# Kernel tuning notes

Hardware: AMD Instinct MI355X
Metric: run time of the kernel (lower is better)

Reference implementation:

```python
import jax, jax.numpy as jnp
import numpy as np

ALPHA = 0.2  # LeakyReLU negative slope
NEG_INF = -9e15


def setup_inputs() -> dict:
    key = jax.random.key(0)
    k1, k2, k3, k4 = jax.random.split(key, 4)
    M, N, Fin, Fout = 32, 1024, 128, 128
    h = jax.random.normal(k1, (M, N, Fin), dtype=jnp.float32)
    adj = jax.random.randint(k2, (M, N, N), 0, 2, dtype=jnp.int32)
    W = jax.random.normal(k3, (Fin, Fout), dtype=jnp.float32) * (1.414 * (6.0 / (Fin + Fout)) ** 0.5)
    a = jax.random.normal(k4, (2 * Fout, 1), dtype=jnp.float32) * (1.414 * (6.0 / (2 * Fout + 1)) ** 0.5)
    return {"h": h, "adj": adj, "W": W, "a": a}


def reference(h, adj, W, a):
    # Wh: [M, N, Fout]
    Wh = jnp.einsum('mnf,fo->mno', h, W)
    Fout = W.shape[1]
    # Algebraic decomposition of concat([Wh_i, Wh_j]) @ a:
    # a_input[m,i,j] @ a == Wh[m,i]@a[:Fout] + Wh[m,j]@a[Fout:]
    e_src = Wh @ a[:Fout, 0]   # [M, N]
    e_dst = Wh @ a[Fout:, 0]   # [M, N]
    e = e_src[:, :, None] + e_dst[:, None, :]      # [M, N, N]
    e = jnp.where(e > 0, e, ALPHA * e)             # LeakyReLU
    masked = jnp.where(adj > 0, e, NEG_INF)
    # NOTE: original softmaxes over dim=1 (faithful reproduction)
    attention = jax.nn.softmax(masked, axis=1)
    # dropout is a no-op in eval mode
    h_prime = jnp.einsum('mij,mjo->mio', attention, Wh)
    return jax.nn.elu(h_prime)  # concat=True branch
```

## Files before the change

### kernel.cpp

```cpp
#include <hip/hip_runtime.h>
#include <hip/hip_bf16.h>

typedef __attribute__((ext_vector_type(4))) float f32x4;
typedef __attribute__((ext_vector_type(8))) short short8;

#define ALPHA 0.2f
#define NEG_BIG -9e15f

static __device__ __forceinline__ short f2bf(float f) {
    __hip_bfloat16 b = __float2bfloat16(f);
    return __builtin_bit_cast(short, b);
}

#define MFMA16(A, B, C) __builtin_amdgcn_mfma_f32_16x16x32_bf16((A), (B), (C), 0, 0, 0)

__global__ __launch_bounds__(128) void k00_wsd(const float* __restrict__ W,
                                               const float* __restrict__ a,
                                               float* __restrict__ wsv,
                                               float* __restrict__ wdv) {
    int k = blockIdx.x, t = threadIdx.x;
    float v = W[k * 128 + t];
    float ps = v * a[t];
    float pd = v * a[128 + t];
    #pragma unroll
    for (int d = 1; d < 64; d <<= 1) {
        ps += __shfl_xor(ps, d);
        pd += __shfl_xor(pd, d);
    }
    __shared__ float tmp[4];
    if ((t & 63) == 0) { tmp[(t >> 6) * 2] = ps; tmp[(t >> 6) * 2 + 1] = pd; }
    __syncthreads();
    if (t == 0) { wsv[k] = tmp[0] + tmp[2]; wdv[k] = tmp[1] + tmp[3]; }
}

__global__ __launch_bounds__(256) void k0_wh(const float* __restrict__ h,
                                             const float* __restrict__ W,
                                             const float* __restrict__ wsv,
                                             const float* __restrict__ wdv,
                                             short* __restrict__ whbt,
                                             float* __restrict__ es,
                                             float* __restrict__ ed) {
    __shared__ __align__(16) short Wt[128 * 136];
    __shared__ __align__(16) float lws[128], lwd[128];
    const int tid = threadIdx.x;
    const int m = blockIdx.x >> 3, rt = blockIdx.x & 7;
    const int R0 = rt * 128;
    #pragma unroll 4
    for (int i = 0; i < 64; ++i) {
        int idx = i * 256 + tid;
        int k = idx >> 7, o = idx & 127;
        Wt[o * 136 + k] = f2bf(W[idx]);
    }
    if (tid < 128) { lws[tid] = wsv[tid]; lwd[tid] = wdv[tid]; }
    __syncthreads();
    const int w = tid >> 6, l = tid & 63;
    const int q = l >> 4, c = l & 15;
    const int row0 = R0 + w * 32 + c;
    f32x4 acc[2][8];
    const f32x4 vzero = {0.f, 0.f, 0.f, 0.f};
    #pragma unroll
    for (int i = 0; i < 2; ++i)
        #pragma unroll
        for (int j = 0; j < 8; ++j) acc[i][j] = vzero;
    float esp0 = 0.f, edp0 = 0.f, esp1 = 0.f, edp1 = 0.f;
    const float* hrow0 = h + ((size_t)m * 1024 + row0) * 128;
    const float* hrow1 = hrow0 + 16 * 128;
    #pragma unroll
    for (int kk = 0; kk < 128; kk += 32) {
        const int kb = kk + q * 8;
        f32x4 wsA = *(const f32x4*)&lws[kb], wsB = *(const f32x4*)&lws[kb + 4];
        f32x4 wdA = *(const f32x4*)&lwd[kb], wdB = *(const f32x4*)&lwd[kb + 4];
        f32x4 h0a = *(const f32x4*)(hrow0 + kb), h0b = *(const f32x4*)(hrow0 + kb + 4);
        f32x4 h1a = *(const f32x4*)(hrow1 + kb), h1b = *(const f32x4*)(hrow1 + kb + 4);
        short8 af0, af1;
        #pragma unroll
        for (int e = 0; e < 4; ++e) {
            esp0 += h0a[e] * wsA[e] + h0b[e] * wsB[e];
            edp0 += h0a[e] * wdA[e] + h0b[e] * wdB[e];
            esp1 += h1a[e] * wsA[e] + h1b[e] * wsB[e];
            edp1 += h1a[e] * wdA[e] + h1b[e] * wdB[e];
            af0[e] = f2bf(h0a[e]); af0[e + 4] = f2bf(h0b[e]);
            af1[e] = f2bf(h1a[e]); af1[e + 4] = f2bf(h1b[e]);
        }
        #pragma unroll
        for (int nf = 0; nf < 8; ++nf) {
            short8 bf = *(const short8*)&Wt[(nf * 16 + c) * 136 + kb];
            acc[0][nf] = MFMA16(af0, bf, acc[0][nf]);
            acc[1][nf] = MFMA16(af1, bf, acc[1][nf]);
        }
    }
    {
        float v0 = esp0; v0 += __shfl_xor(v0, 16); v0 += __shfl_xor(v0, 32);
        float u0 = edp0; u0 += __shfl_xor(u0, 16); u0 += __shfl_xor(u0, 32);
        float v1 = esp1; v1 += __shfl_xor(v1, 16); v1 += __shfl_xor(v1, 32);
        float u1 = edp1; u1 += __shfl_xor(u1, 16); u1 += __shfl_xor(u1, 32);
        if (q == 0) {
            es[m * 1024 + row0] = v0;       ed[m * 1024 + row0] = u0;
            es[m * 1024 + row0 + 16] = v1;  ed[m * 1024 + row0 + 16] = u1;
        }
    }
    #pragma unroll
    for (int mf = 0; mf < 2; ++mf) {
        const int rowb = R0 + w * 32 + mf * 16 + q * 4;
        #pragma unroll
        for (int nf = 0; nf < 8; ++nf) {
            const int o = nf * 16 + c;
            size_t base = ((size_t)m * 128 + o) * 1024 + rowb;
            #pragma unroll
            for (int r = 0; r < 4; r += 2) {
                unsigned lo = (unsigned short)f2bf(acc[mf][nf][r]);
                unsigned hi = (unsigned short)f2bf(acc[mf][nf][r + 1]);
                *(unsigned*)(whbt + base + r) = lo | (hi << 16);
            }
        }
    }
}

__global__ __launch_bounds__(256) void k0m_max(const float* __restrict__ es,
                                               float* __restrict__ mall) {
    const int m = blockIdx.x, tid = threadIdx.x;
    float4 v = *(const float4*)&es[m * 1024 + tid * 4];
    float mx = fmaxf(fmaxf(v.x, v.y), fmaxf(v.z, v.w));
    #pragma unroll
    for (int d = 1; d < 64; d <<= 1) mx = fmaxf(mx, __shfl_xor(mx, d));
    __shared__ float t[4];
    if ((tid & 63) == 0) t[tid >> 6] = mx;
    __syncthreads();
    if (tid == 0) mall[m] = fmaxf(fmaxf(t[0], t[1]), fmaxf(t[2], t[3]));
}

__global__ __launch_bounds__(256) void k1_stats(const int* __restrict__ adj,
                                                const float* __restrict__ es,
                                                const float* __restrict__ ed,
                                                const float* __restrict__ mall,
                                                unsigned long long* __restrict__ bits,
                                                float* __restrict__ spart) {
    const int b = blockIdx.x;
    const int m = b >> 6, it = b & 63;
    const int tid = threadIdx.x;
    const int w = tid >> 6, l = tid & 63;
    const int j0 = tid * 4;
    const float Ma = mall[m];
    const float4 edv = *(const float4*)&ed[m * 1024 + j0];
    float ub[4];
    #pragma unroll
    for (int e = 0; e < 4; ++e) {
        float x = Ma + ((const float*)&edv)[e];
        ub[e] = fmaxf(x, ALPHA * x);
    }
    const int4* ap = (const int4*)(adj + ((size_t)m * 1024 + it * 16) * 1024) + tid;
    int4 av[16];
    #pragma unroll
    for (int r = 0; r < 16; ++r) av[r] = ap[(size_t)r * 256];
    unsigned long long* bp = bits + ((size_t)m * 1024 + it * 16) * 16 + w * 4;
    #pragma unroll
    for (int r = 0; r < 16; ++r) {
        unsigned long long b0 = __ballot(av[r].x != 0);
        unsigned long long b1 = __ballot(av[r].y != 0);
        unsigned long long b2 = __ballot(av[r].z != 0);
        unsigned long long b3 = __ballot(av[r].w != 0);
        if (l == 0) {
            ulonglong2 p0, p1;
            p0.x = b0; p0.y = b1; p1.x = b2; p1.y = b3;
            *(ulonglong2*)(bp + (size_t)r * 16) = p0;
            *(ulonglong2*)(bp + (size_t)r * 16 + 2) = p1;
        }
    }
    float sr[4] = {0.f, 0.f, 0.f, 0.f};
    const float* ep = es + m * 1024 + it * 16;
    #pragma unroll
    for (int r = 0; r < 16; ++r) {
        const float esb = ep[r];
        #pragma unroll
        for (int e = 0; e < 4; ++e) {
            float x = esb + ((const float*)&edv)[e];
            float lk = fmaxf(x, ALPHA * x);
            float t = __expf(lk - ub[e]);
            sr[e] += ((&av[r].x)[e] != 0) ? t : 0.f;
        }
    }
    float4 s4; s4.x = sr[0]; s4.y = sr[1]; s4.z = sr[2]; s4.w = sr[3];
    *(float4*)&spart[((size_t)(m * 64 + it)) * 1024 + j0] = s4;
}

__global__ __launch_bounds__(256) void k1b_combine(const float* __restrict__ spart,
                                                   const float* __restrict__ ed,
                                                   const float* __restrict__ mall,
                                                   float* __restrict__ cc,
                                                   float* __restrict__ dinv) {
    const int g = blockIdx.x * 256 + threadIdx.x;
    const int m = g >> 10, j = g & 1023;
    const float* sp = spart + (size_t)m * 64 * 1024 + j;
    float S = 0.f;
    #pragma unroll
    for (int it = 0; it < 64; ++it) S += sp[it * 1024];
    float x = mall[m] + ed[g];
    float ub = fmaxf(x, ALPHA * x);
    bool dead = !(S > 0.f);
    cc[g] = dead ? NEG_BIG : ub;
    dinv[g] = dead ? (1.0f / 1024.0f) : 1.0f / S;
}

__global__ __launch_bounds__(256) void k2_pv(const unsigned long long* __restrict__ bits,
                                             const short* __restrict__ whbt,
                                             const float* __restrict__ es,
                                             const float* __restrict__ ed,
                                             const float* __restrict__ cc,
                                             const float* __restrict__ dinv,
                                             float* __restrict__ out) {
    __shared__ __align__(16) short Bt[2][128 * 40];
    __shared__ __align__(16) float led[1024], lc[1024], ld[1024];
    const int tid = threadIdx.x;
    const int m = blockIdx.x >> 3, rt = blockIdx.x & 7;
    const int R0 = rt * 128;
    for (int i = tid; i < 1024; i += 256) {
        led[i] = ed[m * 1024 + i];
        lc[i] = cc[m * 1024 + i];
        ld[i] = dinv[m * 1024 + i];
    }
    const int w = tid >> 6, l = tid & 63, q = l >> 4, cl = l & 15;
    const int row0 = R0 + w * 32 + cl;
    const float es0 = es[m * 1024 + row0];
    const float es1 = es[m * 1024 + row0 + 16];
    const unsigned long long* bp0 = bits + ((size_t)m * 1024 + row0) * 16;
    const unsigned long long* bp1 = bp0 + 16 * 16;
    f32x4 acc[2][8];
    const f32x4 vzero = {0.f, 0.f, 0.f, 0.f};
    #pragma unroll
    for (int i = 0; i < 2; ++i)
        #pragma unroll
        for (int jx = 0; jx < 8; ++jx) acc[i][jx] = vzero;
    const int so = tid >> 1, sh = tid & 1;
    const short* gsrc = whbt + ((size_t)m * 128 + so) * 1024 + sh * 16;
    short* dst0 = &Bt[0][so * 40 + sh * 16];
    {
        uint4 r0 = *(const uint4*)gsrc;
        uint4 r1 = *(const uint4*)(gsrc + 8);
        *(uint4*)dst0 = r0;
        *(uint4*)(dst0 + 8) = r1;
    }
    __syncthreads();
    int cur = 0;
    ulonglong2 wa0, wb0, wa1, wb1;
    wa0.x = wa0.y = wb0.x = wb0.y = 0ull;
    wa1.x = wa1.y = wb1.x = wb1.y = 0ull;
    #pragma unroll 2
    for (int kt = 0; kt < 32; ++kt) {
        const int jb = kt * 32 + q * 8;
        if ((kt & 7) == 0) {
            const ulonglong2* q0 = (const ulonglong2*)(bp0 + (kt >> 3) * 4);
            wa0 = q0[0]; wb0 = q0[1];
            const ulonglong2* q1 = (const ulonglong2*)(bp1 + (kt >> 3) * 4);
            wa1 = q1[0]; wb1 = q1[1];
        }
        uint4 n0, n1;
        if (kt < 31) {
            const short* g2 = gsrc + (kt + 1) * 32;
            n0 = *(const uint4*)g2;
            n1 = *(const uint4*)(g2 + 8);
        }
        const f32x4 edA = *(const f32x4*)&led[jb], edB = *(const f32x4*)&led[jb + 4];
        const f32x4 cA = *(const f32x4*)&lc[jb],   cB = *(const f32x4*)&lc[jb + 4];
        const f32x4 dA = *(const f32x4*)&ld[jb],   dB = *(const f32x4*)&ld[jb + 4];
        const int bbase = ((kt & 7) << 3) + (q << 1);
        short8 af0, af1;
        #pragma unroll
        for (int e = 0; e < 8; ++e) {
            const float edv = (e < 4) ? edA[e] : edB[e - 4];
            const float cv = (e < 4) ? cA[e] : cB[e - 4];
            const float dv = (e < 4) ? dA[e] : dB[e - 4];
            const float x0 = es0 + edv, x1 = es1 + edv;
            const float l0 = fmaxf(x0, ALPHA * x0), l1 = fmaxf(x1, ALPHA * x1);
            const int bi = bbase + (e >> 2);
            const unsigned long long q0w = (e & 3) == 0 ? wa0.x : (e & 3) == 1 ? wa0.y
                                         : (e & 3) == 2 ? wb0.x : wb0.y;
            const unsigned long long q1w = (e & 3) == 0 ? wa1.x : (e & 3) == 1 ? wa1.y
                                         : (e & 3) == 2 ? wb1.x : wb1.y;
            const float m0 = ((q0w >> bi) & 1ull) ? l0 : NEG_BIG;
            const float m1 = ((q1w >> bi) & 1ull) ? l1 : NEG_BIG;
            af0[e] = f2bf(__expf(m0 - cv) * dv);
            af1[e] = f2bf(__expf(m1 - cv) * dv);
        }
        const short* bb = &Bt[cur][0];
        #pragma unroll
        for (int nf = 0; nf < 8; ++nf) {
            short8 bf = *(const short8*)&bb[(nf * 16 + cl) * 40 + q * 8];
            acc[0][nf] = MFMA16(af0, bf, acc[0][nf]);
            acc[1][nf] = MFMA16(af1, bf, acc[1][nf]);
        }
        if (kt < 31) {
            short* d2 = &Bt[cur ^ 1][so * 40 + sh * 16];
            *(uint4*)d2 = n0;
            *(uint4*)(d2 + 8) = n1;
            cur ^= 1;
        }
        __syncthreads();
    }
    #pragma unroll
    for (int mf = 0; mf < 2; ++mf) {
        const int rowb = R0 + w * 32 + mf * 16 + q * 4;
        #pragma unroll
        for (int nf = 0; nf < 8; ++nf) {
            const int o = nf * 16 + cl;
            #pragma unroll
            for (int r = 0; r < 4; ++r) {
                const float v = acc[mf][nf][r];
                const float evv = v > 0.f ? v : (__expf(v) - 1.0f);
                out[((size_t)m * 1024 + rowb + r) * 128 + o] = evv;
            }
        }
    }
}

extern "C" void kernel_launch(void* const* d_in, const int* in_sizes, int n_in,
                              void* d_out, int out_size, void* d_ws, size_t ws_size,
                              hipStream_t stream) {
    const float* h = (const float*)d_in[0];
    const int* adj = (const int*)d_in[1];
    const float* W = (const float*)d_in[2];
    const float* a = (const float*)d_in[3];
    float* out = (float*)d_out;

    char* p = (char*)d_ws;
    auto alloc = [&](size_t bytes) -> char* {
        char* r = p;
        p += (bytes + 255) & ~(size_t)255;
        return r;
    };
    short* whbt = (short*)alloc((size_t)32 * 128 * 1024 * 2);
    float* es = (float*)alloc((size_t)32 * 1024 * 4);
    float* ed = (float*)alloc((size_t)32 * 1024 * 4);
    float* wsv = (float*)alloc(128 * 4);
    float* wdv = (float*)alloc(128 * 4);
    float* mall = (float*)alloc(32 * 4);
    unsigned long long* bits = (unsigned long long*)alloc((size_t)32 * 1024 * 16 * 8);
    float* spart = (float*)alloc((size_t)32 * 64 * 1024 * 4);
    float* cc = (float*)alloc((size_t)32 * 1024 * 4);
    float* dinv = (float*)alloc((size_t)32 * 1024 * 4);

    k00_wsd<<<128, 128, 0, stream>>>(W, a, wsv, wdv);
    k0_wh<<<256, 256, 0, stream>>>(h, W, wsv, wdv, whbt, es, ed);
    k0m_max<<<32, 256, 0, stream>>>(es, mall);
    k1_stats<<<2048, 256, 0, stream>>>(adj, es, ed, mall, bits, spart);
    k1b_combine<<<128, 256, 0, stream>>>(spart, ed, mall, cc, dinv);
    k2_pv<<<256, 256, 0, stream>>>(bits, whbt, es, ed, cc, dinv, out);
}
```

Before: 89.21 us.

## Split adjacency bit-packing from softmax column-sum computation into separate kernels

The fused stats kernel is split in two. A pure streaming kernel packs the int32 adjacency into bitmasks, 32 rows per block, with loads batched ahead of the ballots. A second kernel recomputes the column exp-sums from the packed bits, 64 rows per block, with es staged in shared memory. Partial sums shrink from 64 to 16 per column, so the combine step does less work. The cost is an extra launch and a re-read of the bitmask (small) in exchange for decoupling the bandwidth-bound pack from the exp-heavy sum.

New measurement: 99.86 us. +11.9%, slower.

```diff
diff --git a/kernel.cpp b/kernel.cpp
--- a/kernel.cpp
+++ b/kernel.cpp
@@ -129,58 +129,73 @@
     if (tid == 0) mall[m] = fmaxf(fmaxf(t[0], t[1]), fmaxf(t[2], t[3]));
 }
 
-__global__ __launch_bounds__(256) void k1_stats(const int* __restrict__ adj,
+__global__ __launch_bounds__(256) void k1a_pack(const int* __restrict__ adj,
+                                                unsigned long long* __restrict__ bits) {
+    const int b = blockIdx.x;
+    const int m = b >> 5, it = b & 31;
+    const int tid = threadIdx.x, w = tid >> 6, l = tid & 63;
+    const int4* ap = (const int4*)(adj + ((size_t)m * 1024 + it * 32) * 1024) + tid;
+    unsigned long long* bp = bits + ((size_t)m * 1024 + it * 32) * 16 + w * 4;
+    #pragma unroll
+    for (int rb = 0; rb < 32; rb += 16) {
+        int4 av[16];
+        #pragma unroll
+        for (int r = 0; r < 16; ++r) av[r] = ap[(size_t)(rb + r) * 256];
+        __builtin_amdgcn_sched_barrier(0);
+        #pragma unroll
+        for (int r = 0; r < 16; ++r) {
+            unsigned long long b0 = __ballot(av[r].x != 0);
+            unsigned long long b1 = __ballot(av[r].y != 0);
+            unsigned long long b2 = __ballot(av[r].z != 0);
+            unsigned long long b3 = __ballot(av[r].w != 0);
+            if (l == 0) {
+                ulonglong2 p0; p0.x = b0; p0.y = b1;
+                ulonglong2 p1; p1.x = b2; p1.y = b3;
+                *(ulonglong2*)(bp + (size_t)(rb + r) * 16) = p0;
+                *(ulonglong2*)(bp + (size_t)(rb + r) * 16 + 2) = p1;
+            }
+        }
+    }
+}
+
+__global__ __launch_bounds__(256) void k1c_sums(const unsigned long long* __restrict__ bits,
                                                 const float* __restrict__ es,
                                                 const float* __restrict__ ed,
                                                 const float* __restrict__ mall,
-                                                unsigned long long* __restrict__ bits,
                                                 float* __restrict__ spart) {
     const int b = blockIdx.x;
-    const int m = b >> 6, it = b & 63;
-    const int tid = threadIdx.x;
-    const int w = tid >> 6, l = tid & 63;
+    const int m = b >> 4, it = b & 15;
+    const int tid = threadIdx.x, w = tid >> 6, l = tid & 63;
     const int j0 = tid * 4;
+    __shared__ float les[64];
+    if (tid < 64) les[tid] = es[m * 1024 + it * 64 + tid];
     const float Ma = mall[m];
     const float4 edv = *(const float4*)&ed[m * 1024 + j0];
-    float ub[4];
+    float ub[4], sr[4] = {0.f, 0.f, 0.f, 0.f};
     #pragma unroll
     for (int e = 0; e < 4; ++e) {
         float x = Ma + ((const float*)&edv)[e];
         ub[e] = fmaxf(x, ALPHA * x);
     }
-    const int4* ap = (const int4*)(adj + ((size_t)m * 1024 + it * 16) * 1024) + tid;
-    int4 av[16];
-    #pragma unroll
-    for (int r = 0; r < 16; ++r) av[r] = ap[(size_t)r * 256];
-    unsigned long long* bp = bits + ((size_t)m * 1024 + it * 16) * 16 + w * 4;
-    #pragma unroll
-    for (int r = 0; r < 16; ++r) {
-        unsigned long long b0 = __ballot(av[r].x != 0);
-        unsigned long long b1 = __ballot(av[r].y != 0);
-        unsigned long long b2 = __ballot(av[r].z != 0);
-        unsigned long long b3 = __ballot(av[r].w != 0);
-        if (l == 0) {
-            ulonglong2 p0, p1;
-            p0.x = b0; p0.y = b1; p1.x = b2; p1.y = b3;
-            *(ulonglong2*)(bp + (size_t)r * 16) = p0;
-            *(ulonglong2*)(bp + (size_t)r * 16 + 2) = p1;
-        }
-    }
-    float sr[4] = {0.f, 0.f, 0.f, 0.f};
-    const float* ep = es + m * 1024 + it * 16;
-    #pragma unroll
-    for (int r = 0; r < 16; ++r) {
-        const float esb = ep[r];
+    const ulonglong2* bp = (const ulonglong2*)(bits + ((size_t)m * 1024 + it * 64) * 16 + w * 4);
+    __syncthreads();
+    #pragma unroll 4
+    for (int i = 0; i < 64; ++i) {
+        ulonglong2 q0 = bp[i * 8];
+        ulonglong2 q1 = bp[i * 8 + 1];
+        const float esb = les[i];
         #pragma unroll
         for (int e = 0; e < 4; ++e) {
+            const unsigned long long wv = (e == 0) ? q0.x : (e == 1) ? q0.y
+                                        : (e == 2) ? q1.x : q1.y;
             float x = esb + ((const float*)&edv)[e];
             float lk = fmaxf(x, ALPHA * x);
             float t = __expf(lk - ub[e]);
-            sr[e] += ((&av[r].x)[e] != 0) ? t : 0.f;
+            sr[e] += ((wv >> l) & 1ull) ? t : 0.f;
         }
     }
     float4 s4; s4.x = sr[0]; s4.y = sr[1]; s4.z = sr[2]; s4.w = sr[3];
-    *(float4*)&spart[((size_t)(m * 64 + it)) * 1024 + j0] = s4;
+    *(float4*)&spart[((size_t)(m * 16 + it)) * 1024 + j0] = s4;
 }
 
 __global__ __launch_bounds__(256) void k1b_combine(const float* __restrict__ spart,
@@ -190,10 +205,10 @@
                                                    float* __restrict__ dinv) {
     const int g = blockIdx.x * 256 + threadIdx.x;
     const int m = g >> 10, j = g & 1023;
-    const float* sp = spart + (size_t)m * 64 * 1024 + j;
+    const float* sp = spart + (size_t)m * 16 * 1024 + j;
     float S = 0.f;
     #pragma unroll
-    for (int it = 0; it < 64; ++it) S += sp[it * 1024];
+    for (int it = 0; it < 16; ++it) S += sp[it * 1024];
     float x = mall[m] + ed[g];
     float ub = fmaxf(x, ALPHA * x);
     bool dead = !(S > 0.f);
@@ -334,14 +349,15 @@
     float* wdv = (float*)alloc(128 * 4);
     float* mall = (float*)alloc(32 * 4);
     unsigned long long* bits = (unsigned long long*)alloc((size_t)32 * 1024 * 16 * 8);
-    float* spart = (float*)alloc((size_t)32 * 64 * 1024 * 4);
+    float* spart = (float*)alloc((size_t)32 * 16 * 1024 * 4);
     float* cc = (float*)alloc((size_t)32 * 1024 * 4);
     float* dinv = (float*)alloc((size_t)32 * 1024 * 4);
 
     k00_wsd<<<128, 128, 0, stream>>>(W, a, wsv, wdv);
     k0_wh<<<256, 256, 0, stream>>>(h, W, wsv, wdv, whbt, es, ed);
     k0m_max<<<32, 256, 0, stream>>>(es, mall);
-    k1_stats<<<2048, 256, 0, stream>>>(adj, es, ed, mall, bits, spart);
+    k1a_pack<<<1024, 256, 0, stream>>>(adj, bits);
+    k1c_sums<<<512, 256, 0, stream>>>(bits, es, ed, mall, spart);
     k1b_combine<<<128, 256, 0, stream>>>(spart, ed, mall, cc, dinv);
     k2_pv<<<256, 256, 0, stream>>>(bits, whbt, es, ed, cc, dinv, out);
 }
```

## Fuse six GAT kernels into one cooperative persistent kernel with grid syncs

Applied to the files above, without the earlier changes.

Replaces the six-kernel chain with a single cooperative kernel of 256 blocks that runs the Wh projection, the adjacency bitmask/column-sum stats and the attention-times-Wh MFMA phase, separated by grid.sync. Each block recomputes W·a, the column max and the combine step locally instead of running separate small kernels. The adj stream now goes through double-buffered global_load_lds. The aim is to remove launch gaps and the small serial kernels. The cost is that the heavy adj-scan phase runs on only 256 blocks instead of 2048, which may cut bandwidth utilisation.

Result: no change. 88.87 us (-0.4%).

```diff
diff --git a/kernel.cpp b/kernel.cpp
--- a/kernel.cpp
+++ b/kernel.cpp
@@ -1,8 +1,12 @@
 #include <hip/hip_runtime.h>
 #include <hip/hip_bf16.h>
+#include <hip/hip_cooperative_groups.h>
+
+namespace cg = cooperative_groups;
 
 typedef __attribute__((ext_vector_type(4))) float f32x4;
 typedef __attribute__((ext_vector_type(8))) short short8;
+typedef __attribute__((ext_vector_type(4))) int i32x4;
 
 #define ALPHA 0.2f
 #define NEG_BIG -9e15f
@@ -13,6 +17,310 @@
 }
 
 #define MFMA16(A, B, C) __builtin_amdgcn_mfma_f32_16x16x32_bf16((A), (B), (C), 0, 0, 0)
+
+struct SA { short Wt[128 * 136]; float la[256]; float lws[128]; float lwd[128]; };
+struct SB { int buf[2][4096]; float les[128]; float red[8]; };
+struct SC { short Bt[2][128 * 40]; float led[1024]; float lc[1024]; float ld[1024]; float red[8]; };
+
+__global__ __launch_bounds__(256) void gat_mega(
+        const float* __restrict__ h, const int* __restrict__ adj,
+        const float* __restrict__ W, const float* __restrict__ a,
+        short* __restrict__ whbt, float* __restrict__ es, float* __restrict__ ed,
+        unsigned long long* __restrict__ bits, float* __restrict__ spart,
+        float* __restrict__ out) {
+    __shared__ __align__(16) char smem[36864];
+    cg::grid_group grid = cg::this_grid();
+    const int b = blockIdx.x;
+    const int tid = threadIdx.x;
+    const int w = tid >> 6, l = tid & 63;
+    const int q = l >> 4, cl = l & 15;
+    const int m = b >> 3, sub = b & 7;
+    const int T0 = sub * 128;
+
+    {
+        SA* S = (SA*)smem;
+        S->la[tid] = a[tid];
+        __syncthreads();
+        {
+            const int k = tid >> 1, hh = tid & 1;
+            const float* wr = W + k * 128 + hh * 64;
+            float ps = 0.f, pd = 0.f;
+            #pragma unroll
+            for (int f = 0; f < 64; f += 4) {
+                f32x4 wv = *(const f32x4*)(wr + f);
+                #pragma unroll
+                for (int e = 0; e < 4; ++e) {
+                    ps += wv[e] * S->la[hh * 64 + f + e];
+                    pd += wv[e] * S->la[128 + hh * 64 + f + e];
+                }
+            }
+            ps += __shfl_xor(ps, 1);
+            pd += __shfl_xor(pd, 1);
+            if (hh == 0) { S->lws[k] = ps; S->lwd[k] = pd; }
+        }
+        #pragma unroll 4
+        for (int i = 0; i < 64; ++i) {
+            int idx = i * 256 + tid;
+            int kk = idx >> 7, o = idx & 127;
+            S->Wt[o * 136 + kk] = f2bf(W[idx]);
+        }
+        __syncthreads();
+        const int row0 = T0 + w * 32 + cl;
+        f32x4 acc[2][8];
+        const f32x4 vz = {0.f, 0.f, 0.f, 0.f};
+        #pragma unroll
+        for (int i = 0; i < 2; ++i)
+            #pragma unroll
+            for (int j = 0; j < 8; ++j) acc[i][j] = vz;
+        float esp0 = 0.f, edp0 = 0.f, esp1 = 0.f, edp1 = 0.f;
+        const float* hrow0 = h + ((size_t)m * 1024 + row0) * 128;
+        const float* hrow1 = hrow0 + 16 * 128;
+        #pragma unroll
+        for (int kk = 0; kk < 128; kk += 32) {
+            const int kb = kk + q * 8;
+            f32x4 wsA = *(const f32x4*)&S->lws[kb], wsB = *(const f32x4*)&S->lws[kb + 4];
+            f32x4 wdA = *(const f32x4*)&S->lwd[kb], wdB = *(const f32x4*)&S->lwd[kb + 4];
+            f32x4 h0a = *(const f32x4*)(hrow0 + kb), h0b = *(const f32x4*)(hrow0 + kb + 4);
+            f32x4 h1a = *(const f32x4*)(hrow1 + kb), h1b = *(const f32x4*)(hrow1 + kb + 4);
+            short8 af0, af1;
+            #pragma unroll
+            for (int e = 0; e < 4; ++e) {
+                esp0 += h0a[e] * wsA[e] + h0b[e] * wsB[e];
+                edp0 += h0a[e] * wdA[e] + h0b[e] * wdB[e];
+                esp1 += h1a[e] * wsA[e] + h1b[e] * wsB[e];
+                edp1 += h1a[e] * wdA[e] + h1b[e] * wdB[e];
+                af0[e] = f2bf(h0a[e]); af0[e + 4] = f2bf(h0b[e]);
+                af1[e] = f2bf(h1a[e]); af1[e + 4] = f2bf(h1b[e]);
+            }
+            #pragma unroll
+            for (int nf = 0; nf < 8; ++nf) {
+                short8 bf = *(const short8*)&S->Wt[(nf * 16 + cl) * 136 + kb];
+                acc[0][nf] = MFMA16(af0, bf, acc[0][nf]);
+                acc[1][nf] = MFMA16(af1, bf, acc[1][nf]);
+            }
+        }
+        {
+            float v0 = esp0; v0 += __shfl_xor(v0, 16); v0 += __shfl_xor(v0, 32);
+            float u0 = edp0; u0 += __shfl_xor(u0, 16); u0 += __shfl_xor(u0, 32);
+            float v1 = esp1; v1 += __shfl_xor(v1, 16); v1 += __shfl_xor(v1, 32);
+            float u1 = edp1; u1 += __shfl_xor(u1, 16); u1 += __shfl_xor(u1, 32);
+            if (q == 0) {
+                es[m * 1024 + row0] = v0;       ed[m * 1024 + row0] = u0;
+                es[m * 1024 + row0 + 16] = v1;  ed[m * 1024 + row0 + 16] = u1;
+            }
+        }
+        #pragma unroll
+        for (int mf = 0; mf < 2; ++mf) {
+            const int rowb = T0 + w * 32 + mf * 16 + q * 4;
+            #pragma unroll
+            for (int nf = 0; nf < 8; ++nf) {
+                const int o = nf * 16 + cl;
+                size_t base = ((size_t)m * 128 + o) * 1024 + rowb;
+                #pragma unroll
+                for (int r = 0; r < 4; r += 2) {
+                    unsigned lo = (unsigned short)f2bf(acc[mf][nf][r]);
+                    unsigned hi = (unsigned short)f2bf(acc[mf][nf][r + 1]);
+                    *(unsigned*)(whbt + base + r) = lo | (hi << 16);
+                }
+            }
+        }
+    }
+    __threadfence();
+    grid.sync();
+
+    {
+        SB* S = (SB*)smem;
+        {
+            f32x4 ev = *(const f32x4*)&es[m * 1024 + tid * 4];
+            float mx = fmaxf(fmaxf(ev[0], ev[1]), fmaxf(ev[2], ev[3]));
+            #pragma unroll
+            for (int d = 1; d < 64; d <<= 1) mx = fmaxf(mx, __shfl_xor(mx, d));
+            if (l == 0) S->red[w] = mx;
+        }
+        const size_t gr2 = (size_t)m * 1024 + T0;
+        if (tid < 128) S->les[tid] = es[gr2 + tid];
+        __syncthreads();
+        const float Ma = fmaxf(fmaxf(S->red[0], S->red[1]), fmaxf(S->red[2], S->red[3]));
+        const int j0 = tid * 4;
+        const f32x4 edv = *(const f32x4*)&ed[m * 1024 + j0];
+        float ub[4], sr[4] = {0.f, 0.f, 0.f, 0.f};
+        #pragma unroll
+        for (int e = 0; e < 4; ++e) {
+            float x = Ma + edv[e];
+            ub[e] = fmaxf(x, ALPHA * x);
+        }
+        auto issue = [&](int s) {
+            const int row = s * 4 + w;
+            const int* gp = adj + (gr2 + row) * 1024 + l * 4;
+            int* dst = &S->buf[s & 1][w * 1024];
+            #pragma unroll
+            for (int k = 0; k < 4; ++k)
+                __builtin_amdgcn_global_load_lds(
+                    (const __attribute__((address_space(1))) void*)(gp + k * 256),
+                    (__attribute__((address_space(3))) void*)(dst + k * 256), 16, 0, 0);
+        };
+        issue(0);
+        #pragma unroll 1
+        for (int s = 0; s < 32; ++s) {
+            if (s < 31) {
+                issue(s + 1);
+                asm volatile("s_waitcnt vmcnt(16)" ::: "memory");
+            } else {
+                asm volatile("s_waitcnt vmcnt(0)" ::: "memory");
+            }
+            __builtin_amdgcn_s_barrier();
+            const int* bufc = S->buf[s & 1];
+            unsigned long long* bprow = bits + (gr2 + (size_t)s * 4) * 16 + w * 4;
+            #pragma unroll
+            for (int r = 0; r < 4; ++r) {
+                const i32x4 av = *(const i32x4*)&bufc[r * 1024 + j0];
+                unsigned long long b0 = __ballot(av[0] != 0);
+                unsigned long long b1 = __ballot(av[1] != 0);
+                unsigned long long b2 = __ballot(av[2] != 0);
+                unsigned long long b3 = __ballot(av[3] != 0);
+                if (l == 0) {
+                    ulonglong2 p0; p0.x = b0; p0.y = b1;
+                    ulonglong2 p1; p1.x = b2; p1.y = b3;
+                    *(ulonglong2*)(bprow + (size_t)r * 16) = p0;
+                    *(ulonglong2*)(bprow + (size_t)r * 16 + 2) = p1;
+                }
+                const float esb = S->les[s * 4 + r];
+                #pragma unroll
+                for (int e = 0; e < 4; ++e) {
+                    float x = esb + edv[e];
+                    float lk = fmaxf(x, ALPHA * x);
+                    float t = __expf(lk - ub[e]);
+                    sr[e] += (av[e] != 0) ? t : 0.f;
+                }
+            }
+            __builtin_amdgcn_s_barrier();
+        }
+        f32x4 s4; s4[0] = sr[0]; s4[1] = sr[1]; s4[2] = sr[2]; s4[3] = sr[3];
+        *(f32x4*)&spart[((size_t)(m * 8 + sub)) * 1024 + j0] = s4;
+    }
+    __threadfence();
+    grid.sync();
+
+    {
+        SC* S = (SC*)smem;
+        {
+            f32x4 ev = *(const f32x4*)&es[m * 1024 + tid * 4];
+            float mx = fmaxf(fmaxf(ev[0], ev[1]), fmaxf(ev[2], ev[3]));
+            #pragma unroll
+            for (int d = 1; d < 64; d <<= 1) mx = fmaxf(mx, __shfl_xor(mx, d));
+            if (l == 0) S->red[w] = mx;
+        }
+        __syncthreads();
+        const float Ma = fmaxf(fmaxf(S->red[0], S->red[1]), fmaxf(S->red[2], S->red[3]));
+        const int j0 = tid * 4;
+        {
+            f32x4 Sv = {0.f, 0.f, 0.f, 0.f};
+            const float* sp = spart + (size_t)m * 8 * 1024 + j0;
+            #pragma unroll
+            for (int it = 0; it < 8; ++it) Sv += *(const f32x4*)(sp + it * 1024);
+            f32x4 edv4 = *(const f32x4*)&ed[m * 1024 + j0];
+            #pragma unroll
+            for (int e = 0; e < 4; ++e) {
+                float x = Ma + edv4[e];
+                float ubv = fmaxf(x, ALPHA * x);
+                bool dead = !(Sv[e] > 0.f);
+                S->led[j0 + e] = edv4[e];
+                S->lc[j0 + e] = dead ? NEG_BIG : ubv;
+                S->ld[j0 + e] = dead ? (1.0f / 1024.0f) : 1.0f / Sv[e];
+            }
+        }
+        const int row0 = T0 + w * 32 + cl;
+        const float es0 = es[m * 1024 + row0];
+        const float es1 = es[m * 1024 + row0 + 16];
+        const unsigned long long* bp0 = bits + ((size_t)m * 1024 + row0) * 16;
+        const unsigned long long* bp1 = bp0 + 16 * 16;
+        f32x4 acc[2][8];
+        const f32x4 vz = {0.f, 0.f, 0.f, 0.f};
+        #pragma unroll
+        for (int i = 0; i < 2; ++i)
+            #pragma unroll
+            for (int jx = 0; jx < 8; ++jx) acc[i][jx] = vz;
+        const int so = tid >> 1, sh = tid & 1;
+        const short* gsrc = whbt + ((size_t)m * 128 + so) * 1024 + sh * 16;
+        short* dst0 = &S->Bt[0][so * 40 + sh * 16];
+        {
+            uint4 r0 = *(const uint4*)gsrc;
+            uint4 r1 = *(const uint4*)(gsrc + 8);
+            *(uint4*)dst0 = r0;
+            *(uint4*)(dst0 + 8) = r1;
+        }
+        __syncthreads();
+        int cur = 0;
+        ulonglong2 wa0, wb0, wa1, wb1;
+        wa0.x = wa0.y = wb0.x = wb0.y = 0ull;
+        wa1.x = wa1.y = wb1.x = wb1.y = 0ull;
+        #pragma unroll 2
+        for (int kt = 0; kt < 32; ++kt) {
+            const int jb = kt * 32 + q * 8;
+            if ((kt & 7) == 0) {
+                const ulonglong2* q0p = (const ulonglong2*)(bp0 + (kt >> 3) * 4);
+                wa0 = q0p[0]; wb0 = q0p[1];
+                const ulonglong2* q1p = (const ulonglong2*)(bp1 + (kt >> 3) * 4);
+                wa1 = q1p[0]; wb1 = q1p[1];
+            }
+            uint4 n0, n1;
+            if (kt < 31) {
+                const short* g2 = gsrc + (kt + 1) * 32;
+                n0 = *(const uint4*)g2;
+                n1 = *(const uint4*)(g2 + 8);
+            }
+            const f32x4 edA = *(const f32x4*)&S->led[jb], edB = *(const f32x4*)&S->led[jb + 4];
+            const f32x4 cA = *(const f32x4*)&S->lc[jb],   cB = *(const f32x4*)&S->lc[jb + 4];
+            const f32x4 dA = *(const f32x4*)&S->ld[jb],   dB = *(const f32x4*)&S->ld[jb + 4];
+            const int bbase = ((kt & 7) << 3) + (q << 1);
+            short8 af0, af1;
+            #pragma unroll
+            for (int e = 0; e < 8; ++e) {
+                const float edvv = (e < 4) ? edA[e] : edB[e - 4];
+                const float cv = (e < 4) ? cA[e] : cB[e - 4];
+                const float dv = (e < 4) ? dA[e] : dB[e - 4];
+                const float x0 = es0 + edvv, x1 = es1 + edvv;
+                const float l0 = fmaxf(x0, ALPHA * x0), l1 = fmaxf(x1, ALPHA * x1);
+                const int bi = bbase + (e >> 2);
+                const unsigned long long q0w = (e & 3) == 0 ? wa0.x : (e & 3) == 1 ? wa0.y
+                                             : (e & 3) == 2 ? wb0.x : wb0.y;
+                const unsigned long long q1w = (e & 3) == 0 ? wa1.x : (e & 3) == 1 ? wa1.y
+                                             : (e & 3) == 2 ? wb1.x : wb1.y;
+                const float m0 = ((q0w >> bi) & 1ull) ? l0 : NEG_BIG;
+                const float m1 = ((q1w >> bi) & 1ull) ? l1 : NEG_BIG;
+                af0[e] = f2bf(__expf(m0 - cv) * dv);
+                af1[e] = f2bf(__expf(m1 - cv) * dv);
+            }
+            #pragma unroll
+            for (int nf = 0; nf < 8; ++nf) {
+                short8 bf = *(const short8*)&S->Bt[cur][(nf * 16 + cl) * 40 + q * 8];
+                acc[0][nf] = MFMA16(af0, bf, acc[0][nf]);
+                acc[1][nf] = MFMA16(af1, bf, acc[1][nf]);
+            }
+            if (kt < 31) {
+                short* d2 = &S->Bt[cur ^ 1][so * 40 + sh * 16];
+                *(uint4*)d2 = n0;
+                *(uint4*)(d2 + 8) = n1;
+                cur ^= 1;
+            }
+            __syncthreads();
+        }
+        #pragma unroll
+        for (int mf = 0; mf < 2; ++mf) {
+            const int rowb = T0 + w * 32 + mf * 16 + q * 4;
+            #pragma unroll
+            for (int nf = 0; nf < 8; ++nf) {
+                const int o = nf * 16 + cl;
+                #pragma unroll
+                for (int r = 0; r < 4; ++r) {
+                    const float v = acc[mf][nf][r];
+                    const float evv = v > 0.f ? v : (__expf(v) - 1.0f);
+                    out[((size_t)m * 1024 + rowb + r) * 128 + o] = evv;
+                }
+            }
+        }
+    }
+}
 
 __global__ __launch_bounds__(128) void k00_wsd(const float* __restrict__ W,
                                                const float* __restrict__ a,
@@ -338,10 +646,26 @@
     float* cc = (float*)alloc((size_t)32 * 1024 * 4);
     float* dinv = (float*)alloc((size_t)32 * 1024 * 4);
 
-    k00_wsd<<<128, 128, 0, stream>>>(W, a, wsv, wdv);
-    k0_wh<<<256, 256, 0, stream>>>(h, W, wsv, wdv, whbt, es, ed);
-    k0m_max<<<32, 256, 0, stream>>>(es, mall);
-    k1_stats<<<2048, 256, 0, stream>>>(adj, es, ed, mall, bits, spart);
-    k1b_combine<<<128, 256, 0, stream>>>(spart, ed, mall, cc, dinv);
-    k2_pv<<<256, 256, 0, stream>>>(bits, whbt, es, ed, cc, dinv, out);
-}
+    int maxBlk = 0;
+    hipError_t oe = hipOccupancyMaxActiveBlocksPerMultiprocessor(
+        &maxBlk, (const void*)gat_mega, 256, 0);
+    int numCU = 0;
+    hipError_t ae = hipDeviceGetAttribute(&numCU, hipDeviceAttributeMultiprocessorCount, 0);
+    bool useCoop = (oe == hipSuccess) && (ae == hipSuccess) &&
+                   ((long long)maxBlk * numCU >= 256);
+
+    if (useCoop) {
+        void* kargs[] = { (void*)&h, (void*)&adj, (void*)&W, (void*)&a,
+                          (void*)&whbt, (void*)&es, (void*)&ed, (void*)&bits,
+                          (void*)&spart, (void*)&out };
+        hipLaunchCooperativeKernel(reinterpret_cast<void*>(gat_mega), dim3(256), dim3(256),
+                                   kargs, 0, stream);
+    } else {
+        k00_wsd<<<128, 128, 0, stream>>>(W, a, wsv, wdv);
+        k0_wh<<<256, 256, 0, stream>>>(h, W, wsv, wdv, whbt, es, ed);
+        k0m_max<<<32, 256, 0, stream>>>(es, mall);
+        k1_stats<<<2048, 256, 0, stream>>>(adj, es, ed, mall, bits, spart);
+        k1b_combine<<<128, 256, 0, stream>>>(spart, ed, mall, cc, dinv);
+        k2_pv<<<256, 256, 0, stream>>>(bits, whbt, es, ed, cc, dinv, out);
+    }
+}
```
